# Optimization experiments

Measured on AMD Instinct MI355X. Metric: run time of the kernel, lower is better.

The kernel has to match this reference:

```python
import jax, jax.numpy as jnp
import numpy as np

TEMP = 0.07
MOMENTUM = 0.2
K = 8192          # number of sampled negatives per row
NUM_CLASSES = 1000
B, N, D = 256, 32768, 2048
NEG_INF = -1e30


def _gumbel(key, shape):
    u = jax.random.uniform(key, shape, minval=1e-6, maxval=1.0)
    return -jnp.log(-jnp.log(u))


def setup_inputs() -> dict:
    key = jax.random.key(0)
    k1, k2, k3, k4, k5 = jax.random.split(key, 5)
    f = jax.random.normal(k1, (B, D), dtype=jnp.float32)
    f_nv = jax.random.normal(k2, (B, D), dtype=jnp.float32)
    # warmed-up memory bank (the real module L2-normalizes rows on update)
    features = jax.random.normal(k3, (N, D), dtype=jnp.float32)
    features = features / jnp.linalg.norm(features, axis=1, keepdims=True)
    labels = jax.random.randint(k4, (N,), 0, NUM_CLASSES)
    indexes = jax.random.randint(k5, (B,), 0, N)
    return {"f": f, "f_nv": f_nv, "features": features,
            "labels": labels, "indexes": indexes}


def reference(f, f_nv, features, labels, indexes):
    rkey = jax.random.key(42)
    kg1, kg2, kg3 = jax.random.split(rkey, 3)
    k = features                                   # [N, D] memory bank snapshot
    bsz = f.shape[0]

    # l_pos = <f_nv_i, k[indexes_i]>
    l_pos = jnp.sum(f_nv * k[indexes], axis=1, keepdims=True)   # [B, 1]

    mat = jnp.matmul(f, k.T)                       # [B, N]
    mat_sim = jnp.matmul(f_nv, k.T)                # [B, N]

    batch_labels = labels[indexes]                 # [B]
    pos_mask = labels[None, :] == batch_labels[:, None]         # [B, N]

    # torch.randperm-based sampling -> vectorized masked Gumbel sampling.
    # argmax of gumbel restricted to mask = uniform draw from masked set;
    # top-K of gumbel restricted to complement = K draws w/o replacement.
    g1 = _gumbel(kg1, (bsz, k.shape[0]))
    g2 = _gumbel(kg2, (bsz, k.shape[0]))
    g3 = _gumbel(kg3, (bsz, k.shape[0]))

    pos_idx_wogan = jnp.argmax(jnp.where(pos_mask, g1, NEG_INF), axis=1)
    positives_wogan = jnp.take_along_axis(mat, pos_idx_wogan[:, None], axis=1)  # [B,1]

    pos_idx = jnp.argmax(jnp.where(pos_mask, g2, NEG_INF), axis=1)
    positives = jnp.take_along_axis(mat_sim, pos_idx[:, None], axis=1)          # [B,1]

    _, neg_idx = jax.lax.top_k(jnp.where(pos_mask, NEG_INF, g3), K)             # [B,K]
    negatives = jnp.take_along_axis(mat_sim, neg_idx, axis=1)                   # [B,K]

    def ce_target0(logits):
        # CrossEntropyLoss with all targets == 0
        return -jax.nn.log_softmax(logits, axis=1)[:, 0].mean()

    self_out = jnp.concatenate([l_pos, negatives], axis=1) / TEMP
    inter_out = jnp.concatenate([positives, negatives], axis=1) / TEMP
    inter_out_wogan = jnp.concatenate([positives_wogan, negatives], axis=1) / TEMP

    memory_loss = ce_target0(self_out) + ce_target0(inter_out) + ce_target0(inter_out_wogan)

    # no-grad momentum update of the bank (F.normalize uses eps=1e-12)
    upd = MOMENTUM * k[indexes] + (1.0 - MOMENTUM) * f
    upd = upd / jnp.maximum(jnp.linalg.norm(upd, axis=1, keepdims=True), 1e-12)
    new_features = jax.lax.stop_gradient(features.at[indexes].set(upd))

    return memory_loss, new_features
```

## Files before the change

### kernel.cpp

```cpp
#include <hip/hip_runtime.h>
#include <stdint.h>

#define TEMP      0.07f
#define BATCH     256
#define NROWS     32768
#define DIM       2048
#define KNEG      8192

typedef __attribute__((ext_vector_type(8))) short bf16x8;
typedef __attribute__((ext_vector_type(4))) float f32x4;

__host__ __device__ inline void tf2x32(uint32_t ka, uint32_t kb,
                                       uint32_t x0, uint32_t x1,
                                       uint32_t& o0, uint32_t& o1) {
  uint32_t ks2 = ka ^ kb ^ 0x1BD11BDAu;
#define TFR(r) { x0 += x1; x1 = (x1 << r) | (x1 >> (32 - r)); x1 ^= x0; }
  x0 += ka; x1 += kb;
  TFR(13) TFR(15) TFR(26) TFR(6)
  x0 += kb;  x1 += ks2 + 1u;
  TFR(17) TFR(29) TFR(16) TFR(24)
  x0 += ks2; x1 += ka + 2u;
  TFR(13) TFR(15) TFR(26) TFR(6)
  x0 += ka;  x1 += kb + 3u;
  TFR(17) TFR(29) TFR(16) TFR(24)
  x0 += kb;  x1 += ks2 + 4u;
  TFR(13) TFR(15) TFR(26) TFR(6)
  x0 += ks2; x1 += ka + 5u;
#undef TFR
  o0 = x0; o1 = x1;
}

__device__ inline uint32_t ubits_at(uint32_t ka, uint32_t kb, uint32_t q) {
  uint32_t a, b; tf2x32(ka, kb, 0u, q, a, b);
  return (a ^ b) >> 9;
}

__device__ inline float block_sum(float v, float* sm) {
  __syncthreads();
  const int lane = threadIdx.x & 63;
  const int w = threadIdx.x >> 6;
  const int nw = blockDim.x >> 6;
  for (int o = 32; o; o >>= 1) v += __shfl_down(v, o, 64);
  if (lane == 0) sm[w] = v;
  __syncthreads();
  if (w == 0) {
    float x = (lane < nw) ? sm[lane] : 0.f;
    for (int o = 8; o; o >>= 1) x += __shfl_down(x, o, 64);
    if (lane == 0) sm[0] = x;
  }
  __syncthreads();
  return sm[0];
}

__device__ inline uint32_t pk2(float a, float b) {
  uint32_t ua = __float_as_uint(a), ub = __float_as_uint(b);
  ua = (ua + 0x7FFFu + ((ua >> 16) & 1u)) >> 16;
  ub = (ub + 0x7FFFu + ((ub >> 16) & 1u)) >> 16;
  return ua | (ub << 16);
}

__global__ __launch_bounds__(256) void cvtA(const float* __restrict__ A,
                                            uint32_t* __restrict__ Abf) {
  const int t = threadIdx.x;
  const int w = blockIdx.x * 4 + (t >> 6);
  const int l = t & 63;
  const int mt = w >> 6, kt = w & 63;
  const float* src = &A[(size_t)(mt * 16 + (l & 15)) * DIM + kt * 32 + (l >> 4) * 8];
  float4 f0 = *(const float4*)src;
  float4 f1 = *(const float4*)(src + 4);
  *(uint4*)(Abf + (size_t)w * 256 + l * 4) =
      make_uint4(pk2(f0.x, f0.y), pk2(f0.z, f0.w), pk2(f1.x, f1.y), pk2(f1.z, f1.w));
}

__device__ inline void gll16(const float* g, float* l) {
  __builtin_amdgcn_global_load_lds(
      (const __attribute__((address_space(1))) uint32_t*)g,
      (__attribute__((address_space(3))) uint32_t*)l, 16, 0, 0);
}

#define NKS (DIM / 64)

__global__ __launch_bounds__(256, 3) void gemm_tile(
    const uint32_t* __restrict__ Abf,
    const float* __restrict__ Bfeat,
    float* __restrict__ C,
    float* __restrict__ outF,
    int skip) {
  __shared__ float Bs[128 * 64];
  const int t = threadIdx.x;
  const int l = t & 63, w = t >> 6;
  const int bm = blockIdx.x & 1;
  const int bn = blockIdx.x >> 1;
  const int wr = w >> 1, wc = w & 1;
  const bool doCopy = (bm == 0);

  f32x4 acc[4][4] = {};

  for (int t0 = 0; t0 < NKS; ++t0) {
    const int k0 = t0 * 64;
    __syncthreads();
#pragma unroll
    for (int i = 0; i < 8; ++i) {
      const int ii = w * 8 + i;
      const int r = 4 * ii + (l >> 4);
      const int g = (l & 15) ^ ((r & 7) << 1);
      gll16(&Bfeat[(size_t)(bn * 128 + r) * DIM + k0 + g * 4], &Bs[ii * 256]);
    }
    __syncthreads();
    if (doCopy) {
#pragma unroll
      for (int i = 0; i < 8; ++i) {
        const int G = i * 256 + t;
        const int gr = bn * 128 + (G >> 4);
        const size_t off = (size_t)gr * DIM + k0 + (G & 15) * 4;
        f32x4 v = *(const f32x4*)&Bfeat[off];
        if (gr >= skip)
          __builtin_nontemporal_store(v, (f32x4*)&outF[off]);
      }
    }
#pragma unroll
    for (int kk = 0; kk < 2; ++kk) {
      bf16x8 af[4];
#pragma unroll
      for (int m = 0; m < 4; ++m)
        af[m] = *(const bf16x8*)(Abf +
            ((size_t)((bm * 8 + wr * 4 + m) * 64 + t0 * 2 + kk) * 64 + l) * 4);
      bf16x8 bfr[4];
#pragma unroll
      for (int n = 0; n < 4; ++n) {
        const int row = wc * 64 + n * 16 + (l & 15);
        const int e = (2 * (kk * 4 + (l >> 4))) ^ ((row & 7) << 1);
        const float* bp = &Bs[row * 64 + e * 4];
        f32x4 lo = *(const f32x4*)bp;
        f32x4 hi = *(const f32x4*)(bp + 4);
        uint32_t c0, c1, c2, c3;
        asm("v_cvt_pk_bf16_f32 %0, %1, %2" : "=v"(c0) : "v"(lo[0]), "v"(lo[1]));
        asm("v_cvt_pk_bf16_f32 %0, %1, %2" : "=v"(c1) : "v"(lo[2]), "v"(lo[3]));
        asm("v_cvt_pk_bf16_f32 %0, %1, %2" : "=v"(c2) : "v"(hi[0]), "v"(hi[1]));
        asm("v_cvt_pk_bf16_f32 %0, %1, %2" : "=v"(c3) : "v"(hi[2]), "v"(hi[3]));
        union { uint32_t u[4]; bf16x8 b; } cv;
        cv.u[0] = c0; cv.u[1] = c1; cv.u[2] = c2; cv.u[3] = c3;
        bfr[n] = cv.b;
      }
#pragma unroll
      for (int m = 0; m < 4; ++m)
#pragma unroll
        for (int n = 0; n < 4; ++n)
          acc[m][n] = __builtin_amdgcn_mfma_f32_16x16x32_bf16(
              af[m], bfr[n], acc[m][n], 0, 0, 0);
    }
  }

#pragma unroll
  for (int m = 0; m < 4; ++m)
#pragma unroll
    for (int n = 0; n < 4; ++n) {
      const int row0 = bm * 128 + wr * 64 + m * 16 + (l >> 4) * 4;
      const int col = bn * 128 + wc * 64 + n * 16 + (l & 15);
#pragma unroll
      for (int r = 0; r < 4; ++r)
        C[(size_t)(row0 + r) * NROWS + col] = acc[m][n][r];
    }
}

__global__ __launch_bounds__(1024) void sample_loss(
    const float* __restrict__ f, const float* __restrict__ f_nv,
    const float* __restrict__ features, const int* __restrict__ labels,
    const int* __restrict__ indexes, const float* __restrict__ mat_sim,
    float* __restrict__ row_loss,
    uint32_t k1a, uint32_t k1b, uint32_t k2a, uint32_t k2b,
    uint32_t k3a, uint32_t k3b) {
  __shared__ uint32_t keys[NROWS];
  __shared__ uint32_t hist4[4][256];
  __shared__ uint32_t hist[256];
  __shared__ unsigned long long am1, am2;
  __shared__ int tie_j[128];
  __shared__ int tie_cnt;
  __shared__ float sred[16];
  __shared__ float swm[16], sws[16];
  __shared__ uint32_t bc_prefix, bc_rem;
  __shared__ int blab_s;

  const int t = threadIdx.x;
  const int i = blockIdx.x;
  const size_t mbase = (size_t)i * NROWS;

  if (t == 0) {
    blab_s = labels[indexes[i]];
    am1 = 0ull; am2 = 0ull; tie_cnt = 0;
  }
  ((uint32_t*)hist4)[t] = 0u;
  __syncthreads();
  const int blab = blab_s;
  const int hsel = t >> 8;

#pragma unroll 2
  for (int s = 0; s < NROWS / 1024; ++s) {
    int j = t + 1024 * s;
    uint32_t q = (uint32_t)i * NROWS + (uint32_t)j;
    int lab = labels[j];
    uint32_t key;
    if (lab == blab) {
      key = 0u;
      unsigned long long lo = (unsigned long long)(uint32_t)(NROWS - 1 - j);
      uint32_t u1 = ubits_at(k1a, k1b, q);
      uint32_t u2 = ubits_at(k2a, k2b, q);
      atomicMax(&am1, ((unsigned long long)u1 << 32) | lo);
      atomicMax(&am2, ((unsigned long long)u2 << 32) | lo);
    } else {
      key = ubits_at(k3a, k3b, q);
    }
    keys[j] = key;
    atomicAdd(&hist4[hsel][key >> 15], 1u);
  }
  __syncthreads();

  const int jw = NROWS - 1 - (int)(unsigned)(am1 & 0xFFFFFFFFull);
  const int jp = NROWS - 1 - (int)(unsigned)(am2 & 0xFFFFFFFFull);

  const int bank = indexes[i];
  float d1 = 0.f, d2 = 0.f, d3 = 0.f;
  for (int d = t; d < DIM; d += 1024) {
    float fnv = f_nv[(size_t)i * DIM + d];
    d1 += fnv * features[(size_t)bank * DIM + d];
    d2 += f[(size_t)i * DIM + d] * features[(size_t)jw * DIM + d];
    d3 += fnv * features[(size_t)jp * DIM + d];
  }
  const float l_pos = block_sum(d1, sred);
  const float posw  = block_sum(d2, sred);
  const float posv  = block_sum(d3, sred);

  uint32_t prefix = 0, remaining = KNEG;
  const int shifts[3] = {15, 7, 0};
  const int nbits[3]  = {8, 8, 7};
  for (int p = 0; p < 3; ++p) {
    const int sh = shifts[p];
    const int nb = 1 << nbits[p];
    if (p) {
      ((uint32_t*)hist4)[t] = 0u;
      __syncthreads();
      for (int s = 0; s < NROWS / 1024; ++s) {
        int j = t + 1024 * s;
        uint32_t k = keys[j];
        if ((k >> (sh + nbits[p])) == prefix)
          atomicAdd(&hist4[hsel][(k >> sh) & (uint32_t)(nb - 1)], 1u);
      }
    }
    __syncthreads();
    if (t < nb) hist[t] = hist4[0][t] + hist4[1][t] + hist4[2][t] + hist4[3][t];
    __syncthreads();
    if (t == 0) {
      uint32_t c = 0; int b = nb - 1;
      for (;; --b) {
        c += hist[b];
        if (c >= remaining || b == 0) break;
      }
      bc_prefix = (prefix << nbits[p]) | (uint32_t)b;
      bc_rem = remaining - (c - hist[b]);
    }
    __syncthreads();
    prefix = bc_prefix; remaining = bc_rem;
  }
  const uint32_t T = prefix;
  const uint32_t need = remaining;

  float m = -INFINITY, ssum = 0.f;
  for (int s = 0; s < NROWS / 1024; ++s) {
    int j = t + 1024 * s;
    uint32_t k = keys[j];
    if (k > T) {
      float v = mat_sim[mbase + j] / TEMP;
      if (v <= m) ssum += expf(v - m);
      else { ssum = ssum * expf(m - v) + 1.0f; m = v; }
    } else if (k == T) {
      int p = atomicAdd(&tie_cnt, 1);
      if (p < 128) tie_j[p] = j;
    }
  }
  for (int o = 32; o; o >>= 1) {
    float m2 = __shfl_down(m, o, 64);
    float s2 = __shfl_down(ssum, o, 64);
    if (m2 > m) { ssum = ssum * expf(m - m2) + s2; m = m2; }
    else if (m2 != -INFINITY) ssum += s2 * expf(m2 - m);
  }
  if ((t & 63) == 0) { swm[t >> 6] = m; sws[t >> 6] = ssum; }
  __syncthreads();
  if (t < 64) {
    float mm = (t < 16) ? swm[t] : -INFINITY;
    float ss = (t < 16) ? sws[t] : 0.f;
    for (int o = 8; o; o >>= 1) {
      float m2 = __shfl_down(mm, o, 64);
      float s2 = __shfl_down(ss, o, 64);
      if (m2 > mm) { ss = ss * expf(mm - m2) + s2; mm = m2; }
      else if (m2 != -INFINITY) ss += s2 * expf(m2 - mm);
    }
    if (t == 0) { swm[0] = mm; sws[0] = ss; }
  }
  __syncthreads();

  if (t == 0) {
    float M = swm[0], S = sws[0];
    int tc = tie_cnt;
    if (tc <= 128) {
      for (int a2 = 1; a2 < tc; ++a2) {
        int v = tie_j[a2]; int b2 = a2 - 1;
        while (b2 >= 0 && tie_j[b2] > v) { tie_j[b2 + 1] = tie_j[b2]; --b2; }
        tie_j[b2 + 1] = v;
      }
      for (uint32_t r = 0; r < need; ++r) {
        float v = mat_sim[mbase + tie_j[r]] / TEMP;
        if (v <= M) S += expf(v - M);
        else { S = S * expf(M - v) + 1.0f; M = v; }
      }
    } else {
      uint32_t taken = 0;
      for (int j = 0; j < NROWS && taken < need; ++j) {
        if (keys[j] == T) {
          float v = mat_sim[mbase + j] / TEMP;
          if (v <= M) S += expf(v - M);
          else { S = S * expf(M - v) + 1.0f; M = v; }
          ++taken;
        }
      }
    }
    float lp = l_pos / TEMP, pv = posv / TEMP, pw = posw / TEMP;
    float L = 0.f;
    { float X = fmaxf(M, lp); L += X + logf(expf(lp - X) + S * expf(M - X)) - lp; }
    { float X = fmaxf(M, pv); L += X + logf(expf(pv - X) + S * expf(M - X)) - pv; }
    { float X = fmaxf(M, pw); L += X + logf(expf(pw - X) + S * expf(M - X)) - pw; }
    row_loss[i] = L;
  }
}

__global__ void finalize_loss(const float* __restrict__ row_loss,
                              float* __restrict__ out) {
  __shared__ float sm[4];
  int t = threadIdx.x;
  float v = row_loss[t];
  for (int o = 32; o; o >>= 1) v += __shfl_down(v, o, 64);
  if ((t & 63) == 0) sm[t >> 6] = v;
  __syncthreads();
  if (t == 0) out[0] = (sm[0] + sm[1] + sm[2] + sm[3]) * (1.0f / BATCH);
}

__global__ void copy_front(const float* __restrict__ src,
                           float* __restrict__ dst, int n4) {
  int idx = blockIdx.x * blockDim.x + threadIdx.x;
  int stride = gridDim.x * blockDim.x;
  for (int i = idx; i < n4; i += stride) {
    f32x4 v = *(const f32x4*)&src[(size_t)i * 4];
    float* d = &dst[(size_t)i * 4];
    d[0] = v[0]; d[1] = v[1]; d[2] = v[2]; d[3] = v[3];
  }
}

__global__ __launch_bounds__(256) void update_rows(
    const float* __restrict__ f, const float* __restrict__ features,
    const int* __restrict__ indexes, float* __restrict__ outF) {
  __shared__ float sred[16];
  const int i = blockIdx.x;
  const int row = indexes[i];
  for (int i2 = i + 1; i2 < BATCH; ++i2)
    if (indexes[i2] == row) return;
  const int t = threadIdx.x;
  float ss = 0.f;
  for (int d = t; d < DIM; d += 256) {
    float u = 0.2f * features[(size_t)row * DIM + d] + 0.8f * f[(size_t)i * DIM + d];
    ss += u * u;
  }
  ss = block_sum(ss, sred);
  float nrm = fmaxf(sqrtf(ss), 1e-12f);
  for (int d = t; d < DIM; d += 256) {
    float u = 0.2f * features[(size_t)row * DIM + d] + 0.8f * f[(size_t)i * DIM + d];
    outF[(size_t)row * DIM + d] = u / nrm;
  }
}

extern "C" void kernel_launch(void* const* d_in, const int* in_sizes, int n_in,
                              void* d_out, int out_size, void* d_ws, size_t ws_size,
                              hipStream_t stream) {
  (void)in_sizes; (void)n_in; (void)out_size;
  const float* f        = (const float*)d_in[0];
  const float* f_nv     = (const float*)d_in[1];
  const float* features = (const float*)d_in[2];
  const int*   labels   = (const int*)d_in[3];
  const int*   indexes  = (const int*)d_in[4];
  float* out = (float*)d_out;

  const size_t need = ((size_t)BATCH * NROWS + 256 + 262144) * sizeof(float);
  float* mat_sim;
  float* row_loss;
  uint32_t* Abf;
  int skip_rows;
  bool use_ws = (d_ws != nullptr) && (ws_size >= need);
  if (use_ws) {
    mat_sim = (float*)d_ws;
    row_loss = mat_sim + (size_t)BATCH * NROWS;
    Abf = (uint32_t*)(row_loss + 256);
    skip_rows = 0;
  } else {
    mat_sim = out + 4;
    row_loss = mat_sim + (size_t)BATCH * NROWS;
    Abf = (uint32_t*)(row_loss + 256);
    skip_rows = 4352;
  }

  uint32_t c[6];
  { uint32_t a, b;
    tf2x32(0u, 42u, 0u, 0u, a, b); c[0] = a; c[1] = b;
    tf2x32(0u, 42u, 0u, 1u, a, b); c[2] = a; c[3] = b;
    tf2x32(0u, 42u, 0u, 2u, a, b); c[4] = a; c[5] = b; }

  cvtA<<<dim3(256), dim3(256), 0, stream>>>(f_nv, Abf);
  gemm_tile<<<dim3(2 * NROWS / 128), dim3(256), 0, stream>>>(
      Abf, features, mat_sim, out + 1, skip_rows);
  sample_loss<<<dim3(BATCH), dim3(1024), 0, stream>>>(
      f, f_nv, features, labels, indexes, mat_sim, row_loss,
      c[0], c[1], c[2], c[3], c[4], c[5]);
  finalize_loss<<<dim3(1), dim3(256), 0, stream>>>(row_loss, out);
  if (!use_ws) {
    copy_front<<<dim3(2048), dim3(256), 0, stream>>>(
        features, out + 1, 4352 * DIM / 4);
  }
  update_rows<<<dim3(BATCH), dim3(256), 0, stream>>>(f, features, indexes, out + 1);
}
```

Before: 340.6 us.

## Split GEMM and bank copy into separate block roles with full-M 64-column tiles

The GEMM kernel becomes a role-split kernel. Two of every three blocks only stream-copy 32 rows each of the feature bank to the output, and the third computes a full 256x64 output tile of mat_sim. Previously each 128-column tile was computed by two blocks, one per half of M, so each bank row was read twice, and the copy was interleaved with the MMA loop in half of the blocks. The new layout reads each bank slice once for the GEMM, shrinks LDS so occupancy can rise to four blocks per SM, and removes copy work from the compute path, at the cost of a smaller N tile and an extra bank read by the copy blocks.

```diff
diff --git a/kernel.cpp b/kernel.cpp
--- a/kernel.cpp
+++ b/kernel.cpp
@@ -78,61 +78,61 @@
       (__attribute__((address_space(3))) uint32_t*)l, 16, 0, 0);
 }
 
-#define NKS (DIM / 64)
-
-__global__ __launch_bounds__(256, 3) void gemm_tile(
+__global__ __launch_bounds__(256, 4) void mega(
     const uint32_t* __restrict__ Abf,
     const float* __restrict__ Bfeat,
     float* __restrict__ C,
     float* __restrict__ outF,
     int skip) {
-  __shared__ float Bs[128 * 64];
+  __shared__ float Bs[64 * 64];
+  const int role = blockIdx.x % 3;
+  const int g = blockIdx.x / 3;
   const int t = threadIdx.x;
+
+  if (role < 2) {
+    const int r0 = g * 64 + role * 32;
+    const float* src = Bfeat + (size_t)r0 * DIM;
+    float* dst = outF + (size_t)r0 * DIM;
+    const int total4 = 32 * DIM / 4;
+#pragma unroll 4
+    for (int i = t; i < total4; i += 256) {
+      const int gr = r0 + (i >> 9);
+      f32x4 v = *(const f32x4*)(src + (size_t)i * 4);
+      if (gr >= skip)
+        __builtin_nontemporal_store(v, (f32x4*)(dst + (size_t)i * 4));
+    }
+    return;
+  }
+
   const int l = t & 63, w = t >> 6;
-  const int bm = blockIdx.x & 1;
-  const int bn = blockIdx.x >> 1;
-  const int wr = w >> 1, wc = w & 1;
-  const bool doCopy = (bm == 0);
-
   f32x4 acc[4][4] = {};
 
-  for (int t0 = 0; t0 < NKS; ++t0) {
-    const int k0 = t0 * 64;
+  for (int t0 = 0; t0 < DIM / 64; ++t0) {
     __syncthreads();
 #pragma unroll
-    for (int i = 0; i < 8; ++i) {
-      const int ii = w * 8 + i;
+    for (int i = 0; i < 4; ++i) {
+      const int ii = w * 4 + i;
       const int r = 4 * ii + (l >> 4);
-      const int g = (l & 15) ^ ((r & 7) << 1);
-      gll16(&Bfeat[(size_t)(bn * 128 + r) * DIM + k0 + g * 4], &Bs[ii * 256]);
+      const int gs = (l & 15) ^ (r & 7);
+      gll16(&Bfeat[(size_t)(g * 64 + r) * DIM + t0 * 64 + gs * 4],
+            &Bs[ii * 256]);
     }
     __syncthreads();
-    if (doCopy) {
-#pragma unroll
-      for (int i = 0; i < 8; ++i) {
-        const int G = i * 256 + t;
-        const int gr = bn * 128 + (G >> 4);
-        const size_t off = (size_t)gr * DIM + k0 + (G & 15) * 4;
-        f32x4 v = *(const f32x4*)&Bfeat[off];
-        if (gr >= skip)
-          __builtin_nontemporal_store(v, (f32x4*)&outF[off]);
-      }
-    }
 #pragma unroll
     for (int kk = 0; kk < 2; ++kk) {
       bf16x8 af[4];
 #pragma unroll
       for (int m = 0; m < 4; ++m)
         af[m] = *(const bf16x8*)(Abf +
-            ((size_t)((bm * 8 + wr * 4 + m) * 64 + t0 * 2 + kk) * 64 + l) * 4);
+            ((size_t)((w * 4 + m) * 64 + t0 * 2 + kk) * 64 + l) * 4);
       bf16x8 bfr[4];
 #pragma unroll
       for (int n = 0; n < 4; ++n) {
-        const int row = wc * 64 + n * 16 + (l & 15);
-        const int e = (2 * (kk * 4 + (l >> 4))) ^ ((row & 7) << 1);
-        const float* bp = &Bs[row * 64 + e * 4];
-        f32x4 lo = *(const f32x4*)bp;
-        f32x4 hi = *(const f32x4*)(bp + 4);
+        const int row = n * 16 + (l & 15);
+        const int b2 = 2 * (kk * 4 + (l >> 4));
+        const int s = row & 7;
+        f32x4 lo = *(const f32x4*)&Bs[row * 64 + (b2 ^ s) * 4];
+        f32x4 hi = *(const f32x4*)&Bs[row * 64 + ((b2 + 1) ^ s) * 4];
         uint32_t c0, c1, c2, c3;
         asm("v_cvt_pk_bf16_f32 %0, %1, %2" : "=v"(c0) : "v"(lo[0]), "v"(lo[1]));
         asm("v_cvt_pk_bf16_f32 %0, %1, %2" : "=v"(c1) : "v"(lo[2]), "v"(lo[3]));
@@ -155,8 +155,8 @@
   for (int m = 0; m < 4; ++m)
 #pragma unroll
     for (int n = 0; n < 4; ++n) {
-      const int row0 = bm * 128 + wr * 64 + m * 16 + (l >> 4) * 4;
-      const int col = bn * 128 + wc * 64 + n * 16 + (l & 15);
+      const int row0 = w * 64 + m * 16 + (l >> 4) * 4;
+      const int col = g * 64 + n * 16 + (l & 15);
 #pragma unroll
       for (int r = 0; r < 4; ++r)
         C[(size_t)(row0 + r) * NROWS + col] = acc[m][n][r];
@@ -412,7 +412,7 @@
     tf2x32(0u, 42u, 0u, 2u, a, b); c[4] = a; c[5] = b; }
 
   cvtA<<<dim3(256), dim3(256), 0, stream>>>(f_nv, Abf);
-  gemm_tile<<<dim3(2 * NROWS / 128), dim3(256), 0, stream>>>(
+  mega<<<dim3(3 * NROWS / 64), dim3(256), 0, stream>>>(
       Abf, features, mat_sim, out + 1, skip_rows);
   sample_loss<<<dim3(BATCH), dim3(1024), 0, stream>>>(
       f, f_nv, features, labels, indexes, mat_sim, row_loss,
```

Measured after the change: 284.5 us. 1.2x faster.

## Pre-convert feature bank to bf16 in a separate copy pass before GEMM

Applied to the files above, without the earlier changes.

Adds a prep kernel that streams the fp32 feature bank once, writing the new_features copy and a bf16 copy of the bank. The GEMM then loads bf16 tiles into LDS, which halves its B-operand traffic, and drops the in-loop fp32→bf16 conversion and the fused copy. In exchange there is an extra full pass that writes and rereads a 128MB bf16 buffer. The workspace layout and the fallback skip-row count change to fit the new buffer.

```diff
diff --git a/kernel.cpp b/kernel.cpp
--- a/kernel.cpp
+++ b/kernel.cpp
@@ -72,52 +72,50 @@
       make_uint4(pk2(f0.x, f0.y), pk2(f0.z, f0.w), pk2(f1.x, f1.y), pk2(f1.z, f1.w));
 }
 
-__device__ inline void gll16(const float* g, float* l) {
+__global__ __launch_bounds__(256) void prep(const float* __restrict__ src,
+                                            float* __restrict__ outF,
+                                            uint32_t* __restrict__ fbf16,
+                                            int skip) {
+  const int stride = gridDim.x * blockDim.x;
+  const int total = NROWS * DIM / 4;
+  for (int i = blockIdx.x * blockDim.x + threadIdx.x; i < total; i += stride) {
+    f32x4 v = *(const f32x4*)(src + (size_t)i * 4);
+    uint2 b = make_uint2(pk2(v[0], v[1]), pk2(v[2], v[3]));
+    *(uint2*)(fbf16 + (size_t)i * 2) = b;
+    if ((i >> 9) >= skip)
+      __builtin_nontemporal_store(v, (f32x4*)(outF + (size_t)i * 4));
+  }
+}
+
+__device__ inline void gll16(const uint32_t* g, uint32_t* l) {
   __builtin_amdgcn_global_load_lds(
       (const __attribute__((address_space(1))) uint32_t*)g,
       (__attribute__((address_space(3))) uint32_t*)l, 16, 0, 0);
 }
 
-#define NKS (DIM / 64)
-
-__global__ __launch_bounds__(256, 3) void gemm_tile(
+__global__ __launch_bounds__(256, 3) void gemm_bf(
     const uint32_t* __restrict__ Abf,
-    const float* __restrict__ Bfeat,
-    float* __restrict__ C,
-    float* __restrict__ outF,
-    int skip) {
-  __shared__ float Bs[128 * 64];
+    const uint32_t* __restrict__ fbf16,
+    float* __restrict__ C) {
+  __shared__ uint32_t Bs[128 * 32];
   const int t = threadIdx.x;
   const int l = t & 63, w = t >> 6;
   const int bm = blockIdx.x & 1;
   const int bn = blockIdx.x >> 1;
   const int wr = w >> 1, wc = w & 1;
-  const bool doCopy = (bm == 0);
 
   f32x4 acc[4][4] = {};
 
-  for (int t0 = 0; t0 < NKS; ++t0) {
-    const int k0 = t0 * 64;
+  for (int t0 = 0; t0 < DIM / 64; ++t0) {
     __syncthreads();
 #pragma unroll
-    for (int i = 0; i < 8; ++i) {
-      const int ii = w * 8 + i;
-      const int r = 4 * ii + (l >> 4);
-      const int g = (l & 15) ^ ((r & 7) << 1);
-      gll16(&Bfeat[(size_t)(bn * 128 + r) * DIM + k0 + g * 4], &Bs[ii * 256]);
+    for (int i = 0; i < 4; ++i) {
+      const int r = (w * 4 + i) * 8 + (l >> 3);
+      const int g = (l & 7) ^ (r & 7);
+      gll16(&fbf16[(size_t)(bn * 128 + r) * (DIM / 2) + t0 * 32 + g * 4],
+            &Bs[(w * 4 + i) * 256]);
     }
     __syncthreads();
-    if (doCopy) {
-#pragma unroll
-      for (int i = 0; i < 8; ++i) {
-        const int G = i * 256 + t;
-        const int gr = bn * 128 + (G >> 4);
-        const size_t off = (size_t)gr * DIM + k0 + (G & 15) * 4;
-        f32x4 v = *(const f32x4*)&Bfeat[off];
-        if (gr >= skip)
-          __builtin_nontemporal_store(v, (f32x4*)&outF[off]);
-      }
-    }
 #pragma unroll
     for (int kk = 0; kk < 2; ++kk) {
       bf16x8 af[4];
@@ -128,19 +126,9 @@
       bf16x8 bfr[4];
 #pragma unroll
       for (int n = 0; n < 4; ++n) {
-        const int row = wc * 64 + n * 16 + (l & 15);
-        const int e = (2 * (kk * 4 + (l >> 4))) ^ ((row & 7) << 1);
-        const float* bp = &Bs[row * 64 + e * 4];
-        f32x4 lo = *(const f32x4*)bp;
-        f32x4 hi = *(const f32x4*)(bp + 4);
-        uint32_t c0, c1, c2, c3;
-        asm("v_cvt_pk_bf16_f32 %0, %1, %2" : "=v"(c0) : "v"(lo[0]), "v"(lo[1]));
-        asm("v_cvt_pk_bf16_f32 %0, %1, %2" : "=v"(c1) : "v"(lo[2]), "v"(lo[3]));
-        asm("v_cvt_pk_bf16_f32 %0, %1, %2" : "=v"(c2) : "v"(hi[0]), "v"(hi[1]));
-        asm("v_cvt_pk_bf16_f32 %0, %1, %2" : "=v"(c3) : "v"(hi[2]), "v"(hi[3]));
-        union { uint32_t u[4]; bf16x8 b; } cv;
-        cv.u[0] = c0; cv.u[1] = c1; cv.u[2] = c2; cv.u[3] = c3;
-        bfr[n] = cv.b;
+        const int R = wc * 64 + n * 16 + (l & 15);
+        const int slot = (kk * 4 + (l >> 4)) ^ (R & 7);
+        bfr[n] = *(const bf16x8*)&Bs[R * 32 + slot * 4];
       }
 #pragma unroll
       for (int m = 0; m < 4; ++m)
@@ -387,23 +375,24 @@
   const int*   indexes  = (const int*)d_in[4];
   float* out = (float*)d_out;
 
-  const size_t need = ((size_t)BATCH * NROWS + 256 + 262144) * sizeof(float);
+  const size_t n_mat = (size_t)BATCH * NROWS;
+  const size_t n_scratch = n_mat + 256 + 262144 + (size_t)NROWS * DIM / 2;
   float* mat_sim;
   float* row_loss;
   uint32_t* Abf;
+  uint32_t* fbf16;
   int skip_rows;
-  bool use_ws = (d_ws != nullptr) && (ws_size >= need);
+  bool use_ws = (d_ws != nullptr) && (ws_size >= n_scratch * sizeof(float));
   if (use_ws) {
     mat_sim = (float*)d_ws;
-    row_loss = mat_sim + (size_t)BATCH * NROWS;
-    Abf = (uint32_t*)(row_loss + 256);
     skip_rows = 0;
   } else {
     mat_sim = out + 4;
-    row_loss = mat_sim + (size_t)BATCH * NROWS;
-    Abf = (uint32_t*)(row_loss + 256);
-    skip_rows = 4352;
-  }
+    skip_rows = 12544;
+  }
+  row_loss = mat_sim + n_mat;
+  Abf = (uint32_t*)(row_loss + 256);
+  fbf16 = Abf + 262144;
 
   uint32_t c[6];
   { uint32_t a, b;
@@ -412,15 +401,15 @@
     tf2x32(0u, 42u, 0u, 2u, a, b); c[4] = a; c[5] = b; }
 
   cvtA<<<dim3(256), dim3(256), 0, stream>>>(f_nv, Abf);
-  gemm_tile<<<dim3(2 * NROWS / 128), dim3(256), 0, stream>>>(
-      Abf, features, mat_sim, out + 1, skip_rows);
+  prep<<<dim3(2048), dim3(256), 0, stream>>>(features, out + 1, fbf16, skip_rows);
+  gemm_bf<<<dim3(2 * NROWS / 128), dim3(256), 0, stream>>>(Abf, fbf16, mat_sim);
   sample_loss<<<dim3(BATCH), dim3(1024), 0, stream>>>(
       f, f_nv, features, labels, indexes, mat_sim, row_loss,
       c[0], c[1], c[2], c[3], c[4], c[5]);
   finalize_loss<<<dim3(1), dim3(256), 0, stream>>>(row_loss, out);
   if (!use_ws) {
     copy_front<<<dim3(2048), dim3(256), 0, stream>>>(
-        features, out + 1, 4352 * DIM / 4);
+        features, out + 1, 12544 * DIM / 4);
   }
   update_rows<<<dim3(BATCH), dim3(256), 0, stream>>>(f, features, indexes, out + 1);
 }
```

Measured after the change: 329.9 us. 1.03x faster.
